# Kernel optimization log

Hardware: AMD Instinct MI355X
Metric: run time of the kernel (lower is better)

## Reference

```python
import jax, jax.numpy as jnp
import numpy as np

B, N, C, H = 4, 2048, 1024, 16
HD = C // H
SCALE = HD ** -0.5


def setup_inputs() -> dict:
    key = jax.random.key(0)
    k1, k2, k3, k4 = jax.random.split(key, 4)
    x = jax.random.normal(k1, (B, N, C), dtype=jnp.float32)
    # torch nn.Linear weights: [out, in]
    w_qkv = jax.random.normal(k2, (3 * C, C), dtype=jnp.float32) * (C ** -0.5)
    w_proj = jax.random.normal(k3, (C, C), dtype=jnp.float32) * (C ** -0.5)
    b_proj = jax.random.normal(k4, (C,), dtype=jnp.float32) * 0.01
    return {"x": x, "w_qkv": w_qkv, "w_proj": w_proj, "b_proj": b_proj}


def reference(x, w_qkv, w_proj, b_proj):
    Bx, Nx, Cx = x.shape
    # qkv projection: [B,N,3C] -> [3,B,H,N,HD]
    qkv = jnp.einsum('bnc,dc->bnd', x, w_qkv)
    qkv = qkv.reshape(Bx, Nx, 3, H, HD).transpose(2, 0, 3, 1, 4)
    q, k, v = qkv[0], qkv[1], qkv[2]
    attn = jnp.einsum('bhqd,bhkd->bhqk', q, k) * SCALE
    attn = jax.nn.softmax(attn, axis=-1)
    # dropout p=0.0 (eval/identity)
    out = jnp.einsum('bhqk,bhkd->bhqd', attn, v)
    out = out.transpose(0, 2, 1, 3).reshape(Bx, Nx, Cx)
    return jnp.einsum('bnc,dc->bnd', out, w_proj) + b_proj
```

## Files before the change

kernel.cpp:

```cpp
#include <hip/hip_runtime.h>


typedef float f32x2 __attribute__((ext_vector_type(2)));
typedef float f32x4 __attribute__((ext_vector_type(4)));
typedef float f32x16 __attribute__((ext_vector_type(16)));
typedef __bf16 bf16x8 __attribute__((ext_vector_type(8)));
typedef __bf16 bf16x4 __attribute__((ext_vector_type(4)));
typedef __bf16 bf16x2 __attribute__((ext_vector_type(2)));
typedef unsigned int u32;
typedef unsigned int u32x2 __attribute__((ext_vector_type(2)));

__device__ __forceinline__ void async16(const void* g, void* l) {
  __builtin_amdgcn_global_load_lds((const __attribute__((address_space(1))) unsigned int*)g,
                                   (__attribute__((address_space(3))) unsigned int*)l, 16, 0, 0);
}
__device__ __forceinline__ u32 cvtpk_bf16(float lo, float hi) {
  u32 r;
  asm("v_cvt_pk_bf16_f32 %0, %1, %2" : "=v"(r) : "v"(lo), "v"(hi));
  return r;
}
__device__ __forceinline__ void swap32(u32& a, u32& b) {
  asm volatile("v_permlane32_swap_b32 %0, %1" : "+v"(a), "+v"(b));
}
__device__ __forceinline__ float xmax64(float x) { return fmaxf(x, __shfl_xor(x, 32, 64)); }
__device__ __forceinline__ float exp2v(float x) { return __builtin_amdgcn_exp2f(x); }
__device__ __forceinline__ f32x2 pkmax(f32x2 a, f32x2 b) {
  return f32x2{ fmaxf(a.x, b.x), fmaxf(a.y, b.y) };
}

__global__ __launch_bounds__(256) void cast_to_bf16(const float* __restrict__ x,
                                                    const float* __restrict__ wq,
                                                    const float* __restrict__ wp,
                                                    __bf16* __restrict__ xo,
                                                    __bf16* __restrict__ wqo,
                                                    __bf16* __restrict__ wpo) {
  long i = (long)blockIdx.x * 256 + threadIdx.x;
  const float* s; __bf16* d; long j;
  if (i < 2097152L)      { s = x;  d = xo;  j = i; }
  else if (i < 2883584L) { s = wq; d = wqo; j = i - 2097152L; }
  else                   { s = wp; d = wpo; j = i - 2883584L; }
  float4 v = ((const float4*)s)[j];
  bf16x4 o = { (__bf16)v.x, (__bf16)v.y, (__bf16)v.z, (__bf16)v.w };
  ((bf16x4*)d)[j] = o;
}

template <int EPI>
__global__ __launch_bounds__(512) void gemm_bt(const __bf16* __restrict__ A,
                                               const __bf16* __restrict__ Bw,
                                               __bf16* __restrict__ Oq,
                                               float* __restrict__ Of,
                                               const float* __restrict__ bias) {
  const int tid = threadIdx.x;
  const int lane = tid & 63, w = tid >> 6;
  const int arow = lane & 15, agrp = lane >> 4;
  const int wm = w >> 2, wn = w & 3;
  const int bm = blockIdx.x, bn = blockIdx.y;
  __shared__ char gsm[65536];
  f32x4 acc[4][2] = {};

  const int row0 = tid >> 3, cc0 = tid & 7;
  const int sc0 = cc0 ^ (row0 & 7);
  const __bf16* Ag0 = A + ((size_t)(bm * 128 + row0) << 10) + sc0 * 8;
  const __bf16* Ag1 = A + ((size_t)(bm * 128 + row0 + 64) << 10) + sc0 * 8;
  const __bf16* Bg0 = Bw + ((size_t)(bn * 128 + row0) << 10) + sc0 * 8;
  const __bf16* Bg1 = Bw + ((size_t)(bn * 128 + row0 + 64) << 10) + sc0 * 8;
  const int ld0 = tid * 16;

#define GSTAGE(buf, kt)                                   \
  {                                                       \
    char* S_ = gsm + (buf) * 32768;                       \
    async16(Ag0 + (kt), S_ + ld0);                        \
    async16(Ag1 + (kt), S_ + 8192 + ld0);                 \
    async16(Bg0 + (kt), S_ + 16384 + ld0);                \
    async16(Bg1 + (kt), S_ + 24576 + ld0);                \
  }

  GSTAGE(0, 0)
  __syncthreads();

  for (int t = 0; t < 16; ++t) {
    if (t < 15) GSTAGE((t + 1) & 1, (t + 1) * 64)
    char* AsB = gsm + (t & 1) * 32768;
    char* BsB = AsB + 16384;
#pragma unroll
    for (int kk = 0; kk < 2; ++kk) {
      bf16x8 af[4], bfr[2];
      const int csw = (kk * 64 + agrp * 16) ^ ((arow & 7) << 4);
#pragma unroll
      for (int mi = 0; mi < 4; ++mi)
        af[mi] = *(const bf16x8*)(AsB + (wm * 64 + mi * 16 + arow) * 128 + csw);
#pragma unroll
      for (int ni = 0; ni < 2; ++ni)
        bfr[ni] = *(const bf16x8*)(BsB + (wn * 32 + ni * 16 + arow) * 128 + csw);
      __builtin_amdgcn_s_setprio(1);
#pragma unroll
      for (int mi = 0; mi < 4; ++mi)
#pragma unroll
        for (int ni = 0; ni < 2; ++ni)
          acc[mi][ni] = __builtin_amdgcn_mfma_f32_16x16x32_bf16(af[mi], bfr[ni], acc[mi][ni], 0, 0, 0);
      __builtin_amdgcn_s_setprio(0);
    }
    __syncthreads();
  }
#undef GSTAGE

  const int rowb = bm * 128 + wm * 64 + agrp * 4;
  const int colb = bn * 128 + wn * 32 + arow;
  if (EPI == 0) {
#pragma unroll
    for (int mi = 0; mi < 4; ++mi) {
      const int row = rowb + mi * 16;
      const int bidx = row >> 11;
#pragma unroll
      for (int ni = 0; ni < 2; ++ni) {
        f32x4 v = acc[mi][ni];
        const int col = colb + ni * 16;
        const int which = col >> 10;
        const int h = (col >> 6) & 15;
        const int hd = col & 63;
        const float s = (which == 0) ? 0.18033688011112042f : 1.0f;
        __bf16* dst = Oq + ((size_t)which * 64 + bidx * 16 + h) * (size_t)(2048 * 64) + hd;
#pragma unroll
        for (int i = 0; i < 4; ++i)
          dst[(size_t)((row + i) & 2047) * 64] = (__bf16)(v[i] * s);
      }
    }
  } else {
#pragma unroll
    for (int mi = 0; mi < 4; ++mi) {
      const int row = rowb + mi * 16;
#pragma unroll
      for (int ni = 0; ni < 2; ++ni) {
        const int col = colb + ni * 16;
        const float bv = bias[col];
        f32x4 v = acc[mi][ni];
#pragma unroll
        for (int i = 0; i < 4; ++i)
          Of[(size_t)(row + i) * 1024 + col] = v[i] + bv;
      }
    }
  }
}

__global__ __launch_bounds__(256) void mhsa_attn(const __bf16* __restrict__ QKV,
                                                 __bf16* __restrict__ Out) {
  const int tid = threadIdx.x;
  const int lane = tid & 63, w = tid >> 6;
  const int blk = blockIdx.x;
  const int bh = blk & 63, qt = blk >> 6;
  const int lq = lane & 31, hi = lane >> 5;
  const int l7 = lane & 7, l3 = lane >> 3;

  const size_t bhoff = (size_t)bh * (2048 * 64);
  const __bf16* Qp = QKV + bhoff;
  const __bf16* Kp = QKV + (size_t)(64 * 2048 * 64) + bhoff;
  const __bf16* Vp = QKV + (size_t)(128 * 2048 * 64) + bhoff;

  __shared__ char smem[32768];

  const int q0 = qt * 128 + w * 32;

  bf16x8 qf[4];
#pragma unroll
  for (int s = 0; s < 4; ++s)
    qf[s] = *(const bf16x8*)&Qp[(size_t)(q0 + lq) * 64 + s * 16 + hi * 8];

  union { u32 wv[4]; bf16x8 v; } ou;
  ou.wv[0] = ou.wv[1] = ou.wv[2] = ou.wv[3] = 0x3F803F80u;
  const bf16x8 onesA = ou.v;

  f32x16 Oacc0 = 0.f, Oacc1 = 0.f;
  f32x16 lacc = 0.f;
  float m_run = -1e30f;

  const __bf16* Kg = Kp + (size_t)(w * 16 + l3) * 64 + ((l7 ^ l3) * 8);
  const int kldoff = w * 2048 + lane * 16;

  const int c8v = tid >> 5, k0v = (tid & 31) * 2;

  {
    async16(Kg, smem + kldoff);
    async16(Kg + 512, smem + kldoff + 1024);
    bf16x8 v0 = *(const bf16x8*)&Vp[(size_t)k0v * 64 + c8v * 8];
    bf16x8 v1 = *(const bf16x8*)&Vp[(size_t)(k0v + 1) * 64 + c8v * 8];
    char* Vb = smem + 8192;
#pragma unroll
    for (int j = 0; j < 8; ++j) {
      const int d = c8v * 8 + j;
      bf16x2 pr = { v0[j], v1[j] };
      *(bf16x2*)(Vb + ((d * 128 + k0v * 2) ^ ((d & 7) << 4))) = pr;
    }
  }
  __syncthreads();

  for (int t = 0; t < 32; ++t) {
    char* Kc = smem + (t & 1) * 16384;
    char* Vc = Kc + 8192;
    char* Kn = smem + ((t & 1) ^ 1) * 16384;
    char* Vn = Kn + 8192;

    bf16x8 v0n, v1n;
    const bool pf = (t < 31);
    if (pf) {
      const size_t ktn = (size_t)(t + 1) * 64;
      async16(Kg + ktn * 64, Kn + kldoff);
      async16(Kg + ktn * 64 + 512, Kn + kldoff + 1024);
      v0n = *(const bf16x8*)&Vp[(ktn + k0v) * 64 + c8v * 8];
      v1n = *(const bf16x8*)&Vp[(ktn + k0v + 1) * 64 + c8v * 8];
    }

    f32x16 st0 = 0.f, st1 = 0.f;
    __builtin_amdgcn_s_setprio(1);
#pragma unroll
    for (int s = 0; s < 4; ++s) {
      bf16x8 kf = *(const bf16x8*)(Kc + lq * 128 + ((s * 32 + hi * 16) ^ (l7 << 4)));
      st0 = __builtin_amdgcn_mfma_f32_32x32x16_bf16(kf, qf[s], st0, 0, 0, 0);
    }
#pragma unroll
    for (int s = 0; s < 4; ++s) {
      bf16x8 kf = *(const bf16x8*)(Kc + (32 + lq) * 128 + ((s * 32 + hi * 16) ^ (l7 << 4)));
      st1 = __builtin_amdgcn_mfma_f32_32x32x16_bf16(kf, qf[s], st1, 0, 0, 0);
    }
    __builtin_amdgcn_s_setprio(0);

    f32x2 m2 = f32x2{ st0[0], st0[1] };
#pragma unroll
    for (int r = 1; r < 8; ++r) m2 = pkmax(m2, f32x2{ st0[2 * r], st0[2 * r + 1] });
#pragma unroll
    for (int r = 0; r < 8; ++r) m2 = pkmax(m2, f32x2{ st1[2 * r], st1[2 * r + 1] });
    float mx = xmax64(fmaxf(m2.x, m2.y));

    if (!__all(mx - m_run <= 8.f)) {
      const float mnew = fmaxf(m_run, mx);
      const float fs = exp2v(m_run - mnew);
      m_run = mnew;
#pragma unroll
      for (int r = 0; r < 16; ++r) { Oacc0[r] *= fs; Oacc1[r] *= fs; lacc[r] *= fs; }
    }

    const float mb = m_run;
#pragma unroll
    for (int r = 0; r < 16; ++r) st0[r] = exp2v(st0[r] - mb);
#pragma unroll
    for (int r = 0; r < 16; ++r) st1[r] = exp2v(st1[r] - mb);

    bf16x8 pa[4];
#pragma unroll
    for (int kb = 0; kb < 2; ++kb) {
      const f32x16& st = kb ? st1 : st0;
#pragma unroll
      for (int s16 = 0; s16 < 2; ++s16) {
        u32 A0 = cvtpk_bf16(st[8 * s16 + 0], st[8 * s16 + 1]);
        u32 B0 = cvtpk_bf16(st[8 * s16 + 4], st[8 * s16 + 5]);
        swap32(A0, B0);
        u32 A1 = cvtpk_bf16(st[8 * s16 + 2], st[8 * s16 + 3]);
        u32 B1 = cvtpk_bf16(st[8 * s16 + 6], st[8 * s16 + 7]);
        swap32(A1, B1);
        union { u32 wv[4]; bf16x8 v; } uu;
        uu.wv[0] = A0; uu.wv[1] = A1; uu.wv[2] = B0; uu.wv[3] = B1;
        pa[kb * 2 + s16] = uu.v;
      }
    }

    __builtin_amdgcn_s_setprio(1);
#pragma unroll
    for (int ks = 0; ks < 4; ++ks) {
      bf16x8 vf = *(const bf16x8*)(Vc + lq * 128 + ((ks * 32 + hi * 16) ^ (l7 << 4)));
      Oacc0 = __builtin_amdgcn_mfma_f32_32x32x16_bf16(vf, pa[ks], Oacc0, 0, 0, 0);
      lacc = __builtin_amdgcn_mfma_f32_32x32x16_bf16(onesA, pa[ks], lacc, 0, 0, 0);
    }
#pragma unroll
    for (int ks = 0; ks < 4; ++ks) {
      bf16x8 vf = *(const bf16x8*)(Vc + (32 + lq) * 128 + ((ks * 32 + hi * 16) ^ (l7 << 4)));
      Oacc1 = __builtin_amdgcn_mfma_f32_32x32x16_bf16(vf, pa[ks], Oacc1, 0, 0, 0);
    }
    __builtin_amdgcn_s_setprio(0);

    if (pf) {
#pragma unroll
      for (int j = 0; j < 8; ++j) {
        const int d = c8v * 8 + j;
        bf16x2 pr = { v0n[j], v1n[j] };
        *(bf16x2*)(Vn + ((d * 128 + k0v * 2) ^ ((d & 7) << 4))) = pr;
      }
    }
    __syncthreads();
  }

  const float inv = 1.0f / lacc[0];
  const int b = bh >> 4, h = bh & 15;
  __bf16* orow = Out + ((size_t)(b * 2048 + q0 + lq)) * 1024 + h * 64;
#pragma unroll
  for (int db = 0; db < 2; ++db) {
    const f32x16& O = db ? Oacc1 : Oacc0;
#pragma unroll
    for (int rg = 0; rg < 4; ++rg) {
      u32 plo = cvtpk_bf16(O[rg * 4 + 0] * inv, O[rg * 4 + 1] * inv);
      u32 phi = cvtpk_bf16(O[rg * 4 + 2] * inv, O[rg * 4 + 3] * inv);
      u32x2 pk = { plo, phi };
      *(u32x2*)&orow[db * 32 + rg * 8 + hi * 4] = pk;
    }
  }
}

extern "C" void kernel_launch(void* const* d_in, const int* in_sizes, int n_in,
                              void* d_out, int out_size, void* d_ws, size_t ws_size,
                              hipStream_t stream) {
  const float* x  = (const float*)d_in[0];
  const float* wq = (const float*)d_in[1];
  const float* wp = (const float*)d_in[2];
  const float* bp = (const float*)d_in[3];
  char* ws = (char*)d_ws;

  __bf16* xo   = (__bf16*)(ws);
  __bf16* wqo  = (__bf16*)(ws + 16777216);
  __bf16* wpo  = (__bf16*)(ws + 23068672);
  __bf16* qkv  = (__bf16*)(ws + 25165824);
  __bf16* aout = xo;
  float* y = (float*)d_out;

  cast_to_bf16<<<12288, 256, 0, stream>>>(x, wq, wp, xo, wqo, wpo);
  gemm_bt<0><<<dim3(64, 24), 512, 0, stream>>>(xo, wqo, qkv, nullptr, nullptr);
  mhsa_attn<<<1024, 256, 0, stream>>>(qkv, aout);
  gemm_bt<1><<<dim3(64, 8), 512, 0, stream>>>(aout, wpo, nullptr, y, bp);
}
```

Measured before the change: 187.7 us.

## Split attention KV range in two with a log-sum-exp merge kernel

Attention now runs over two halves of the key/value sequence in separate blocks, doubling the grid to 2048 blocks. Each block writes a partial normalized output plus a per-row log-sum-exp score, and a new merge kernel combines the two partials with softmax weights. The aim is more parallelism and shorter per-block loops. The cost is extra global traffic for the partial outputs, the scores and the merge pass, plus one more kernel launch. If the workspace is too small, the code falls back to the original single-pass path.

```diff
diff --git a/kernel.cpp b/kernel.cpp
--- a/kernel.cpp
+++ b/kernel.cpp
@@ -143,11 +143,18 @@
 }
 
 __global__ __launch_bounds__(256) void mhsa_attn(const __bf16* __restrict__ QKV,
-                                                 __bf16* __restrict__ Out) {
+                                                 __bf16* __restrict__ P0,
+                                                 __bf16* __restrict__ P1,
+                                                 float* __restrict__ S,
+                                                 const int split) {
   const int tid = threadIdx.x;
   const int lane = tid & 63, w = tid >> 6;
   const int blk = blockIdx.x;
-  const int bh = blk & 63, qt = blk >> 6;
+  const int bh = blk & 63;
+  const int qt = split ? ((blk >> 6) & 15) : (blk >> 6);
+  const int part = split ? (blk >> 10) : 0;
+  const int iters = split ? 16 : 32;
+  const int kvbase = part << 10;
   const int lq = lane & 31, hi = lane >> 5;
   const int l7 = lane & 7, l3 = lane >> 3;
 
@@ -179,10 +186,10 @@
   const int c8v = tid >> 5, k0v = (tid & 31) * 2;
 
   {
-    async16(Kg, smem + kldoff);
-    async16(Kg + 512, smem + kldoff + 1024);
-    bf16x8 v0 = *(const bf16x8*)&Vp[(size_t)k0v * 64 + c8v * 8];
-    bf16x8 v1 = *(const bf16x8*)&Vp[(size_t)(k0v + 1) * 64 + c8v * 8];
+    async16(Kg + (size_t)kvbase * 64, smem + kldoff);
+    async16(Kg + (size_t)(kvbase + 8) * 64, smem + kldoff + 1024);
+    bf16x8 v0 = *(const bf16x8*)&Vp[(size_t)(kvbase + k0v) * 64 + c8v * 8];
+    bf16x8 v1 = *(const bf16x8*)&Vp[(size_t)(kvbase + k0v + 1) * 64 + c8v * 8];
     char* Vb = smem + 8192;
 #pragma unroll
     for (int j = 0; j < 8; ++j) {
@@ -193,16 +200,16 @@
   }
   __syncthreads();
 
-  for (int t = 0; t < 32; ++t) {
+  for (int t = 0; t < iters; ++t) {
     char* Kc = smem + (t & 1) * 16384;
     char* Vc = Kc + 8192;
     char* Kn = smem + ((t & 1) ^ 1) * 16384;
     char* Vn = Kn + 8192;
 
     bf16x8 v0n, v1n;
-    const bool pf = (t < 31);
+    const bool pf = (t < iters - 1);
     if (pf) {
-      const size_t ktn = (size_t)(t + 1) * 64;
+      const size_t ktn = (size_t)(kvbase + (t + 1) * 64);
       async16(Kg + ktn * 64, Kn + kldoff);
       async16(Kg + ktn * 64 + 512, Kn + kldoff + 1024);
       v0n = *(const bf16x8*)&Vp[(ktn + k0v) * 64 + c8v * 8];
@@ -287,9 +294,11 @@
     __syncthreads();
   }
 
-  const float inv = 1.0f / lacc[0];
+  const float lsum = lacc[0];
+  const float inv = 1.0f / lsum;
   const int b = bh >> 4, h = bh & 15;
-  __bf16* orow = Out + ((size_t)(b * 2048 + q0 + lq)) * 1024 + h * 64;
+  __bf16* dstbuf = (split && part) ? P1 : P0;
+  __bf16* orow = dstbuf + ((size_t)(b * 2048 + q0 + lq)) * 1024 + h * 64;
 #pragma unroll
   for (int db = 0; db < 2; ++db) {
     const f32x16& O = db ? Oacc1 : Oacc0;
@@ -301,6 +310,31 @@
       *(u32x2*)&orow[db * 32 + rg * 8 + hi * 4] = pk;
     }
   }
+  if (split) {
+    S[(size_t)part * 131072 + (size_t)bh * 2048 + q0 + lq] = m_run + log2f(lsum);
+  }
+}
+
+__global__ __launch_bounds__(256) void attn_merge(const __bf16* __restrict__ P0,
+                                                  const __bf16* __restrict__ P1,
+                                                  const float* __restrict__ S,
+                                                  __bf16* __restrict__ out) {
+  const int i = blockIdx.x * 256 + threadIdx.x;
+  const int col8 = i & 127;
+  const int q = (i >> 7) & 2047;
+  const int b = i >> 18;
+  const int h = col8 >> 3;
+  const size_t bhq = (size_t)(b * 16 + h) * 2048 + q;
+  const float s0 = S[bhq], s1 = S[131072 + bhq];
+  const float sm = fmaxf(s0, s1);
+  float w0 = exp2v(s0 - sm), w1 = exp2v(s1 - sm);
+  const float inv = 1.0f / (w0 + w1);
+  w0 *= inv; w1 *= inv;
+  bf16x8 a = ((const bf16x8*)P0)[i], c = ((const bf16x8*)P1)[i];
+  bf16x8 o;
+#pragma unroll
+  for (int j = 0; j < 8; ++j) o[j] = (__bf16)((float)a[j] * w0 + (float)c[j] * w1);
+  ((bf16x8*)out)[i] = o;
 }
 
 extern "C" void kernel_launch(void* const* d_in, const int* in_sizes, int n_in,
@@ -316,11 +350,23 @@
   __bf16* wqo  = (__bf16*)(ws + 16777216);
   __bf16* wpo  = (__bf16*)(ws + 23068672);
   __bf16* qkv  = (__bf16*)(ws + 25165824);
-  __bf16* aout = xo;
   float* y = (float*)d_out;
 
   cast_to_bf16<<<12288, 256, 0, stream>>>(x, wq, wp, xo, wqo, wpo);
   gemm_bt<0><<<dim3(64, 24), 512, 0, stream>>>(xo, wqo, qkv, nullptr, nullptr);
-  mhsa_attn<<<1024, 256, 0, stream>>>(qkv, aout);
-  gemm_bt<1><<<dim3(64, 8), 512, 0, stream>>>(aout, wpo, nullptr, y, bp);
-}
+
+  const size_t NEED = 92274688;
+  if (ws_size >= NEED) {
+    __bf16* P0 = xo;
+    __bf16* P1 = (__bf16*)(ws + 75497472);
+    float*  Sv = (float*)(ws + 16777216);
+    __bf16* aout = qkv;
+    mhsa_attn<<<2048, 256, 0, stream>>>(qkv, P0, P1, Sv, 1);
+    attn_merge<<<4096, 256, 0, stream>>>(P0, P1, Sv, aout);
+    gemm_bt<1><<<dim3(64, 8), 512, 0, stream>>>(aout, wpo, nullptr, y, bp);
+  } else {
+    __bf16* aout = xo;
+    mhsa_attn<<<1024, 256, 0, stream>>>(qkv, aout, nullptr, nullptr, 0);
+    gemm_bt<1><<<dim3(64, 8), 512, 0, stream>>>(aout, wpo, nullptr, y, bp);
+  }
+}
```

New measurement: 204.7 us. 9.0% more time.
